# Performance work log

Measured on AMD Instinct MI355X. Metric: run time of the kernel, lower is better.

The kernel has to match this reference:

```python
import jax, jax.numpy as jnp
import numpy as np

TIME_LEN = 8
JOINT_NUM = 22
SEQ = TIME_LEN * JOINT_NUM  # 176
H_NUM = 8
H_DIM = 32
NEG_BIG = -9e15


def _temporal_mask():
    # ones everywhere, except block-diagonal joint x joint blocks zeroed, plus identity
    m = np.ones((SEQ, SEQ), dtype=np.float32)
    for i in range(TIME_LEN):
        m[i * JOINT_NUM:(i + 1) * JOINT_NUM, i * JOINT_NUM:(i + 1) * JOINT_NUM] = 0.0
    spatial = 1.0 - m
    temporal = m + np.eye(SEQ, dtype=np.float32)
    return jnp.asarray(temporal), jnp.asarray(spatial)


def setup_inputs() -> dict:
    key = jax.random.key(0)
    ks = jax.random.split(key, 4)
    B, S, D_in = 256, SEQ, 128
    D_model = H_NUM * H_DIM
    s = 1.0 / np.sqrt(D_in)
    return {
        "x": jax.random.normal(ks[0], (B, S, D_in), dtype=jnp.float32),
        "Wq": jax.random.normal(ks[1], (D_in, D_model), dtype=jnp.float32) * s,
        "bq": jnp.zeros((D_model,), dtype=jnp.float32),
        "Wk": jax.random.normal(ks[2], (D_in, D_model), dtype=jnp.float32) * s,
        "bk": jnp.zeros((D_model,), dtype=jnp.float32),
        "Wv": jax.random.normal(ks[3], (D_in, D_model), dtype=jnp.float32) * s,
        "bv": jnp.zeros((D_model,), dtype=jnp.float32),
    }


def reference(x, Wq, bq, Wk, bk, Wv, bv):
    B = x.shape[0]
    mask, _ = _temporal_mask()  # att_type == 'temporal'

    def split_heads(t):  # [B,S,H*D] -> [B,H,S,D]
        return t.reshape(B, SEQ, H_NUM, H_DIM).transpose(0, 2, 1, 3)

    q = split_heads(x @ Wq + bq)
    k = split_heads(x @ Wk + bk)
    v = split_heads(jax.nn.relu(x @ Wv + bv))  # value map has ReLU

    scores = jnp.einsum("bhsd,bhtd->bhst", q, k) / jnp.sqrt(jnp.float32(H_DIM))
    scores = scores * mask + (1.0 - mask) * NEG_BIG
    att = jax.nn.softmax(scores, axis=-1)
    out = jnp.einsum("bhst,bhtd->bhsd", att, v)
    return out.transpose(0, 2, 1, 3).reshape(B, SEQ, H_NUM * H_DIM)
```

## Files before the change

### kernel.cpp

```cpp
#include <hip/hip_runtime.h>


#define SEQ    176
#define HD     32
#define DIN    128
#define DMODEL 256

#define KSTRIDE 44
#define VSTRIDE 204

typedef unsigned short ushort_t;
typedef __attribute__((ext_vector_type(8))) short short8;
typedef __attribute__((ext_vector_type(4))) short short4v;
typedef __attribute__((ext_vector_type(4))) float float4v;
typedef __attribute__((ext_vector_type(4))) unsigned short ushort4v;

#define WS_WT 0u
#define WS_X  196608u

#define OFF_KS 13056
#define OFF_VT (OFF_KS + 176 * KSTRIDE)
#define SMEM_TOTAL (OFF_VT + 32 * VSTRIDE)

__device__ __forceinline__ ushort_t f2bf(float f) {
    union { float f; unsigned int u; } cv; cv.f = f;
    unsigned int u = cv.u;
    unsigned int rb = 0x7FFFu + ((u >> 16) & 1u);
    return (ushort_t)((u + rb) >> 16);
}

__global__ __launch_bounds__(256)
void k0_conv(const float* __restrict__ x,
             const float* __restrict__ Wq, const float* __restrict__ Wk,
             const float* __restrict__ Wv,
             ushort_t* __restrict__ WT, ushort_t* __restrict__ X16)
{
    int bid = blockIdx.x;
    if (bid < 5632) {
        int f4 = bid * 256 + threadIdx.x;
        float4 v = reinterpret_cast<const float4*>(x)[f4];
        ushort4v o;
        o.x = f2bf(v.x); o.y = f2bf(v.y); o.z = f2bf(v.z); o.w = f2bf(v.w);
        reinterpret_cast<ushort4v*>(X16)[f4] = o;
    } else {
        int idx = (bid - 5632) * 256 + threadIdx.x;
        int e = idx * 4;
        int mat = e >> 15, h = (e >> 12) & 7, n = (e >> 7) & 31, k = e & 127;
        const float* W = (mat == 0) ? Wq : ((mat == 1) ? Wk : Wv);
        ushort4v o;
        o.x = f2bf(W[(k + 0) * DMODEL + h * HD + n]);
        o.y = f2bf(W[(k + 1) * DMODEL + h * HD + n]);
        o.z = f2bf(W[(k + 2) * DMODEL + h * HD + n]);
        o.w = f2bf(W[(k + 3) * DMODEL + h * HD + n]);
        reinterpret_cast<ushort4v*>(WT)[idx] = o;
    }
}

__global__ __launch_bounds__(704, 6)
void k1_attn(const ushort_t* __restrict__ X16, const ushort_t* __restrict__ WT,
             const float* __restrict__ bq, const float* __restrict__ bk,
             const float* __restrict__ bv, float* __restrict__ out)
{
    __shared__ ushort_t smem[SMEM_TOTAL];
    ushort_t* WS = smem;
    ushort_t* KS = smem + OFF_KS;
    ushort_t* VT = smem + OFF_VT;

    const int tid  = threadIdx.x;
    const int lane = tid & 63;
    const int w    = tid >> 6;
    const int c    = lane & 15;
    const int q    = lane >> 4;

    const int xcd = blockIdx.x & 7;
    const int j   = blockIdx.x >> 3;
    const int b   = xcd * 32 + (j >> 3);
    const int h   = j & 7;

#pragma unroll
    for (int it = 0; it < 3; ++it) {
        int c8 = tid + it * 704;
        if (c8 < 1536) {
            int mat = c8 >> 9, rem = c8 & 511, n = rem >> 4, kc = rem & 15;
            short8 v = *reinterpret_cast<const short8*>(
                WT + (size_t)(((mat * 8 + h) * 32 + n) * 128 + kc * 8));
            *reinterpret_cast<short8*>(WS + (mat * 32 + n) * 136 + kc * 8) = v;
        }
    }
    if (tid < 512) {
        VT[(tid >> 4) * VSTRIDE + 176 + (tid & 15)] = 0;
    }
    __syncthreads();

    const ushort_t* xr = X16 + ((size_t)b * SEQ + w * 16 + c) * DIN;
    short8 xf[4];
#pragma unroll
    for (int kk = 0; kk < 4; ++kk)
        xf[kk] = *reinterpret_cast<const short8*>(xr + kk * 32 + q * 8);

    const float qscale = 0.17677669529663687f * 1.4426950408889634f;

    short8 qf8;
#pragma unroll
    for (int nt = 0; nt < 2; ++nt) {
        const ushort_t* wrow = WS + (nt * 16 + c) * 136 + q * 8;
        float4v acc = {0.f, 0.f, 0.f, 0.f};
#pragma unroll
        for (int kk = 0; kk < 4; ++kk) {
            short8 wf = *reinterpret_cast<const short8*>(wrow + kk * 32);
            acc = __builtin_amdgcn_mfma_f32_16x16x32_bf16(wf, xf[kk], acc, 0, 0, 0);
        }
        float4 bb = *reinterpret_cast<const float4*>(bq + h * HD + nt * 16 + q * 4);
        qf8[nt * 4 + 0] = (short)f2bf((acc[0] + bb.x) * qscale);
        qf8[nt * 4 + 1] = (short)f2bf((acc[1] + bb.y) * qscale);
        qf8[nt * 4 + 2] = (short)f2bf((acc[2] + bb.z) * qscale);
        qf8[nt * 4 + 3] = (short)f2bf((acc[3] + bb.w) * qscale);
    }
#pragma unroll
    for (int nt = 0; nt < 2; ++nt) {
        const ushort_t* wrow = WS + (32 + nt * 16 + c) * 136 + q * 8;
        float4v acc = {0.f, 0.f, 0.f, 0.f};
#pragma unroll
        for (int kk = 0; kk < 4; ++kk) {
            short8 wf = *reinterpret_cast<const short8*>(wrow + kk * 32);
            acc = __builtin_amdgcn_mfma_f32_16x16x32_bf16(xf[kk], wf, acc, 0, 0, 0);
        }
        float bia = bk[h * HD + nt * 16 + c];
#pragma unroll
        for (int r = 0; r < 4; ++r)
            KS[(w * 16 + q * 4 + r) * KSTRIDE + nt * 16 + c] = f2bf(acc[r] + bia);
    }
#pragma unroll
    for (int nt = 0; nt < 2; ++nt) {
        const ushort_t* wrow = WS + (64 + nt * 16 + c) * 136 + q * 8;
        float4v acc = {0.f, 0.f, 0.f, 0.f};
#pragma unroll
        for (int kk = 0; kk < 4; ++kk) {
            short8 wf = *reinterpret_cast<const short8*>(wrow + kk * 32);
            acc = __builtin_amdgcn_mfma_f32_16x16x32_bf16(wf, xf[kk], acc, 0, 0, 0);
        }
        float4 bb = *reinterpret_cast<const float4*>(bv + h * HD + nt * 16 + q * 4);
#pragma unroll
        for (int r = 0; r < 4; ++r) {
            float bias_r = (r == 0) ? bb.x : (r == 1) ? bb.y : (r == 2) ? bb.z : bb.w;
            float v = acc[r] + bias_r;
            v = v > 0.f ? v : 0.f;
            VT[(nt * 16 + q * 4 + r) * VSTRIDE + w * 16 + c] = f2bf(v);
        }
    }
    __syncthreads();

    const int t_row = w * 16 + c;
    const int lo = (t_row / 22) * 22;
    float su = 0.f;
    short8 pf[6];
    pf[5] = (short8){0, 0, 0, 0, 0, 0, 0, 0};
#pragma unroll
    for (int n = 0; n < 11; ++n) {
        const ushort_t* krow = KS + (n * 16 + c) * KSTRIDE;
        short4v ka = *reinterpret_cast<const short4v*>(krow + q * 4);
        short4v kb = *reinterpret_cast<const short4v*>(krow + 16 + q * 4);
        short8 kf = {ka.x, ka.y, ka.z, ka.w, kb.x, kb.y, kb.z, kb.w};
        float4v s = {0.f, 0.f, 0.f, 0.f};
        s = __builtin_amdgcn_mfma_f32_16x16x32_bf16(kf, qf8, s, 0, 0, 0);
#pragma unroll
        for (int r = 0; r < 4; ++r) {
            int tp = n * 16 + q * 4 + r;
            float sv = (((unsigned)(tp - lo) < 22u) && (tp != t_row)) ? -1e30f : s[r];
            float e = __builtin_amdgcn_exp2f(sv);
            su += e;
            pf[n >> 1][(n & 1) * 4 + r] = (short)f2bf(e);
        }
    }
    su += __shfl_xor(su, 16, 64);
    su += __shfl_xor(su, 32, 64);
    const float invs = 1.0f / su;

    float* ob = out + ((size_t)b * SEQ + t_row) * DMODEL + h * HD;
#pragma unroll
    for (int mt = 0; mt < 2; ++mt) {
        const ushort_t* vrow = VT + (mt * 16 + c) * VSTRIDE;
        float4v o = {0.f, 0.f, 0.f, 0.f};
#pragma unroll
        for (int g = 0; g < 6; ++g) {
            short4v va = *reinterpret_cast<const short4v*>(vrow + (2 * g) * 16 + q * 4);
            short4v vb = *reinterpret_cast<const short4v*>(vrow + (2 * g + 1) * 16 + q * 4);
            short8 vf = {va.x, va.y, va.z, va.w, vb.x, vb.y, vb.z, vb.w};
            o = __builtin_amdgcn_mfma_f32_16x16x32_bf16(vf, pf[g], o, 0, 0, 0);
        }
        float4 st;
        st.x = o[0] * invs; st.y = o[1] * invs;
        st.z = o[2] * invs; st.w = o[3] * invs;
        *reinterpret_cast<float4*>(ob + mt * 16 + q * 4) = st;
    }
}

extern "C" void kernel_launch(void* const* d_in, const int* in_sizes, int n_in,
                              void* d_out, int out_size, void* d_ws, size_t ws_size,
                              hipStream_t stream) {
    const float* x  = (const float*)d_in[0];
    const float* Wq = (const float*)d_in[1];
    const float* bq = (const float*)d_in[2];
    const float* Wk = (const float*)d_in[3];
    const float* bk = (const float*)d_in[4];
    const float* Wv = (const float*)d_in[5];
    const float* bv = (const float*)d_in[6];
    float* out = (float*)d_out;

    char* ws = (char*)d_ws;
    ushort_t* WT  = (ushort_t*)(ws + WS_WT);
    ushort_t* X16 = (ushort_t*)(ws + WS_X);

    k0_conv<<<dim3(5728), dim3(256), 0, stream>>>(x, Wq, Wk, Wv, WT, X16);
    k1_attn<<<dim3(2048), dim3(704), 0, stream>>>(X16, WT, bq, bk, bv, out);
}
```

Before: 132.2 us.

## Fold Q scale into weights, swap MFMA operands for packed LDS stores

```diff
diff --git a/kernel.cpp b/kernel.cpp
--- a/kernel.cpp
+++ b/kernel.cpp
@@ -8,12 +8,16 @@
 
 #define KSTRIDE 44
 #define VSTRIDE 204
+#define QSCALE  0.25506100344358246f
 
 typedef unsigned short ushort_t;
+typedef unsigned int uint_t;
 typedef __attribute__((ext_vector_type(8))) short short8;
 typedef __attribute__((ext_vector_type(4))) short short4v;
 typedef __attribute__((ext_vector_type(4))) float float4v;
 typedef __attribute__((ext_vector_type(4))) unsigned short ushort4v;
+typedef __attribute__((ext_vector_type(2))) unsigned int uint2v;
+typedef __attribute__((ext_vector_type(4))) unsigned int uint4v;
 
 #define WS_WT 0u
 #define WS_X  196608u
@@ -27,6 +31,9 @@
     unsigned int u = cv.u;
     unsigned int rb = 0x7FFFu + ((u >> 16) & 1u);
     return (ushort_t)((u + rb) >> 16);
+}
+__device__ __forceinline__ uint_t pk2(float a, float b) {
+    return (uint_t)f2bf(a) | ((uint_t)f2bf(b) << 16);
 }
 
 __global__ __launch_bounds__(256)
@@ -47,11 +54,12 @@
         int e = idx * 4;
         int mat = e >> 15, h = (e >> 12) & 7, n = (e >> 7) & 31, k = e & 127;
         const float* W = (mat == 0) ? Wq : ((mat == 1) ? Wk : Wv);
+        const float sc = (mat == 0) ? QSCALE : 1.0f;
         ushort4v o;
-        o.x = f2bf(W[(k + 0) * DMODEL + h * HD + n]);
-        o.y = f2bf(W[(k + 1) * DMODEL + h * HD + n]);
-        o.z = f2bf(W[(k + 2) * DMODEL + h * HD + n]);
-        o.w = f2bf(W[(k + 3) * DMODEL + h * HD + n]);
+        o.x = f2bf(W[(k + 0) * DMODEL + h * HD + n] * sc);
+        o.y = f2bf(W[(k + 1) * DMODEL + h * HD + n] * sc);
+        o.z = f2bf(W[(k + 2) * DMODEL + h * HD + n] * sc);
+        o.w = f2bf(W[(k + 3) * DMODEL + h * HD + n] * sc);
         reinterpret_cast<ushort4v*>(WT)[idx] = o;
     }
 }
@@ -61,7 +69,7 @@
              const float* __restrict__ bq, const float* __restrict__ bk,
              const float* __restrict__ bv, float* __restrict__ out)
 {
-    __shared__ ushort_t smem[SMEM_TOTAL];
+    __shared__ __align__(16) ushort_t smem[SMEM_TOTAL];
     ushort_t* WS = smem;
     ushort_t* KS = smem + OFF_KS;
     ushort_t* VT = smem + OFF_VT;
@@ -76,6 +84,21 @@
     const int j   = blockIdx.x >> 3;
     const int b   = xcd * 32 + (j >> 3);
     const int h   = j & 7;
+
+    const ushort_t* xr = X16 + ((size_t)b * SEQ + w * 16 + c) * DIN;
+    short8 xf[4];
+#pragma unroll
+    for (int kk = 0; kk < 4; ++kk)
+        xf[kk] = *reinterpret_cast<const short8*>(xr + kk * 32 + q * 8);
+
+    float4 bqv0 = *reinterpret_cast<const float4*>(bq + h * HD + q * 4);
+    float4 bqv1 = *reinterpret_cast<const float4*>(bq + h * HD + 16 + q * 4);
+    bqv0.x *= QSCALE; bqv0.y *= QSCALE; bqv0.z *= QSCALE; bqv0.w *= QSCALE;
+    bqv1.x *= QSCALE; bqv1.y *= QSCALE; bqv1.z *= QSCALE; bqv1.w *= QSCALE;
+    float4 bkv0 = *reinterpret_cast<const float4*>(bk + h * HD + q * 4);
+    float4 bkv1 = *reinterpret_cast<const float4*>(bk + h * HD + 16 + q * 4);
+    const float bvc0 = bv[h * HD + c];
+    const float bvc1 = bv[h * HD + 16 + c];
 
 #pragma unroll
     for (int it = 0; it < 3; ++it) {
@@ -92,15 +115,7 @@
     }
     __syncthreads();
 
-    const ushort_t* xr = X16 + ((size_t)b * SEQ + w * 16 + c) * DIN;
-    short8 xf[4];
-#pragma unroll
-    for (int kk = 0; kk < 4; ++kk)
-        xf[kk] = *reinterpret_cast<const short8*>(xr + kk * 32 + q * 8);
-
-    const float qscale = 0.17677669529663687f * 1.4426950408889634f;
-
-    short8 qf8;
+    uint_t qd[4];
 #pragma unroll
     for (int nt = 0; nt < 2; ++nt) {
         const ushort_t* wrow = WS + (nt * 16 + c) * 136 + q * 8;
@@ -110,12 +125,14 @@
             short8 wf = *reinterpret_cast<const short8*>(wrow + kk * 32);
             acc = __builtin_amdgcn_mfma_f32_16x16x32_bf16(wf, xf[kk], acc, 0, 0, 0);
         }
-        float4 bb = *reinterpret_cast<const float4*>(bq + h * HD + nt * 16 + q * 4);
-        qf8[nt * 4 + 0] = (short)f2bf((acc[0] + bb.x) * qscale);
-        qf8[nt * 4 + 1] = (short)f2bf((acc[1] + bb.y) * qscale);
-        qf8[nt * 4 + 2] = (short)f2bf((acc[2] + bb.z) * qscale);
-        qf8[nt * 4 + 3] = (short)f2bf((acc[3] + bb.w) * qscale);
-    }
+        const float4 bb = nt ? bqv1 : bqv0;
+        qd[nt * 2 + 0] = pk2(acc[0] + bb.x, acc[1] + bb.y);
+        qd[nt * 2 + 1] = pk2(acc[2] + bb.z, acc[3] + bb.w);
+    }
+    short8 qf8;
+    { union { uint4v u; short8 s; } t;
+      t.u = (uint4v){qd[0], qd[1], qd[2], qd[3]}; qf8 = t.s; }
+
 #pragma unroll
     for (int nt = 0; nt < 2; ++nt) {
         const ushort_t* wrow = WS + (32 + nt * 16 + c) * 136 + q * 8;
@@ -123,12 +140,13 @@
 #pragma unroll
         for (int kk = 0; kk < 4; ++kk) {
             short8 wf = *reinterpret_cast<const short8*>(wrow + kk * 32);
-            acc = __builtin_amdgcn_mfma_f32_16x16x32_bf16(xf[kk], wf, acc, 0, 0, 0);
-        }
-        float bia = bk[h * HD + nt * 16 + c];
-#pragma unroll
-        for (int r = 0; r < 4; ++r)
-            KS[(w * 16 + q * 4 + r) * KSTRIDE + nt * 16 + c] = f2bf(acc[r] + bia);
+            acc = __builtin_amdgcn_mfma_f32_16x16x32_bf16(wf, xf[kk], acc, 0, 0, 0);
+        }
+        const float4 bb = nt ? bkv1 : bkv0;
+        uint2v kd;
+        kd.x = pk2(acc[0] + bb.x, acc[1] + bb.y);
+        kd.y = pk2(acc[2] + bb.z, acc[3] + bb.w);
+        *reinterpret_cast<uint2v*>(&KS[(w * 16 + c) * KSTRIDE + nt * 16 + q * 4]) = kd;
     }
 #pragma unroll
     for (int nt = 0; nt < 2; ++nt) {
@@ -137,24 +155,25 @@
 #pragma unroll
         for (int kk = 0; kk < 4; ++kk) {
             short8 wf = *reinterpret_cast<const short8*>(wrow + kk * 32);
-            acc = __builtin_amdgcn_mfma_f32_16x16x32_bf16(wf, xf[kk], acc, 0, 0, 0);
-        }
-        float4 bb = *reinterpret_cast<const float4*>(bv + h * HD + nt * 16 + q * 4);
-#pragma unroll
-        for (int r = 0; r < 4; ++r) {
-            float bias_r = (r == 0) ? bb.x : (r == 1) ? bb.y : (r == 2) ? bb.z : bb.w;
-            float v = acc[r] + bias_r;
-            v = v > 0.f ? v : 0.f;
-            VT[(nt * 16 + q * 4 + r) * VSTRIDE + w * 16 + c] = f2bf(v);
-        }
+            acc = __builtin_amdgcn_mfma_f32_16x16x32_bf16(xf[kk], wf, acc, 0, 0, 0);
+        }
+        const float bb = nt ? bvc1 : bvc0;
+        float v0 = acc[0] + bb; v0 = v0 > 0.f ? v0 : 0.f;
+        float v1 = acc[1] + bb; v1 = v1 > 0.f ? v1 : 0.f;
+        float v2 = acc[2] + bb; v2 = v2 > 0.f ? v2 : 0.f;
+        float v3 = acc[3] + bb; v3 = v3 > 0.f ? v3 : 0.f;
+        uint2v vd;
+        vd.x = pk2(v0, v1);
+        vd.y = pk2(v2, v3);
+        *reinterpret_cast<uint2v*>(&VT[(nt * 16 + c) * VSTRIDE + w * 16 + q * 4]) = vd;
     }
     __syncthreads();
 
     const int t_row = w * 16 + c;
     const int lo = (t_row / 22) * 22;
     float su = 0.f;
-    short8 pf[6];
-    pf[5] = (short8){0, 0, 0, 0, 0, 0, 0, 0};
+    uint_t pw[24];
+    pw[22] = 0u; pw[23] = 0u;
 #pragma unroll
     for (int n = 0; n < 11; ++n) {
         const ushort_t* krow = KS + (n * 16 + c) * KSTRIDE;
@@ -163,14 +182,16 @@
         short8 kf = {ka.x, ka.y, ka.z, ka.w, kb.x, kb.y, kb.z, kb.w};
         float4v s = {0.f, 0.f, 0.f, 0.f};
         s = __builtin_amdgcn_mfma_f32_16x16x32_bf16(kf, qf8, s, 0, 0, 0);
+        float e[4];
 #pragma unroll
         for (int r = 0; r < 4; ++r) {
             int tp = n * 16 + q * 4 + r;
             float sv = (((unsigned)(tp - lo) < 22u) && (tp != t_row)) ? -1e30f : s[r];
-            float e = __builtin_amdgcn_exp2f(sv);
-            su += e;
-            pf[n >> 1][(n & 1) * 4 + r] = (short)f2bf(e);
-        }
+            e[r] = __builtin_amdgcn_exp2f(sv);
+            su += e[r];
+        }
+        pw[n * 2 + 0] = pk2(e[0], e[1]);
+        pw[n * 2 + 1] = pk2(e[2], e[3]);
     }
     su += __shfl_xor(su, 16, 64);
     su += __shfl_xor(su, 32, 64);
@@ -184,9 +205,11 @@
 #pragma unroll
         for (int g = 0; g < 6; ++g) {
             short4v va = *reinterpret_cast<const short4v*>(vrow + (2 * g) * 16 + q * 4);
-            short4v vb = *reinterpret_cast<const short4v*>(vrow + (2 * g + 1) * 16 + q * 4);
-            short8 vf = {va.x, va.y, va.z, va.w, vb.x, vb.y, vb.z, vb.w};
-            o = __builtin_amdgcn_mfma_f32_16x16x32_bf16(vf, pf[g], o, 0, 0, 0);
+            short4v vb2 = *reinterpret_cast<const short4v*>(vrow + (2 * g + 1) * 16 + q * 4);
+            short8 vf = {va.x, va.y, va.z, va.w, vb2.x, vb2.y, vb2.z, vb2.w};
+            union { uint4v u; short8 s; } pt;
+            pt.u = (uint4v){pw[4 * g], pw[4 * g + 1], pw[4 * g + 2], pw[4 * g + 3]};
+            o = __builtin_amdgcn_mfma_f32_16x16x32_bf16(vf, pt.s, o, 0, 0, 0);
         }
         float4 st;
         st.x = o[0] * invs; st.y = o[1] * invs;
```

New measurement: 134.3 us. Within noise of the previous version (+1.6%).
